# Kernel optimization log

Measured on AMD Instinct MI355X. Metric: run time of the kernel, lower is better.

## Reference

```python
import jax, jax.numpy as jnp
import numpy as np

HIDDEN = [256, 128, 64, 32]
N_IN, N_OUT = 784, 10
V_REST = 0.0; V_RESET = 0.0; V_TH = 1.0; R_MEM = 1.0; DT = 1.0; TAU = 2.0
ALPHA = DT / TAU
SLOPE = 5.0
B, T = 128, 500


def setup_inputs() -> dict:
    key = jax.random.key(0)
    ks = jax.random.split(key, 7)
    sizes = [N_IN] + HIDDEN + [N_OUT]
    inp = {"input_spikes": jax.random.uniform(ks[0], (B, N_IN, T), dtype=jnp.float32)}
    for i in range(len(sizes) - 1):  # 5 weight matrices
        inp[f"w{i}"] = jax.random.uniform(ks[i + 1], (sizes[i], sizes[i + 1]), dtype=jnp.float32) * 0.1
    return inp


def _lif(v, cur):
    # voltage update, surrogate spike, hard reset (reset uses detached spike)
    v = v + (-(v - V_REST) + R_MEM * cur) * ALPHA
    s = jax.nn.sigmoid(SLOPE * (v - V_TH))
    sd = jax.lax.stop_gradient(s)
    v = v * (1.0 - sd) + V_RESET * sd
    return v, s


def reference(input_spikes, w0, w1, w2, w3, w4):
    ws = [jax.nn.relu(w) for w in (w0, w1, w2, w3, w4)]
    n_h = len(HIDDEN)
    b = input_spikes.shape[0]
    dt = input_spikes.dtype
    xs = jnp.transpose(input_spikes, (2, 0, 1))  # (T, B, N_IN)

    v0 = tuple(jnp.full((b, h), V_REST, dtype=dt) for h in HIDDEN)
    v_out0 = jnp.full((b, N_OUT), V_REST, dtype=dt)
    s_prev0 = tuple(jnp.zeros((b, h), dtype=dt) for h in HIDDEN)

    def step(carry, x_t):
        vs, v_out, s_prev = carry
        new_vs, new_s = [], []
        # layer 0 driven by current-step input
        v, s = _lif(vs[0], x_t @ ws[0])
        new_vs.append(v); new_s.append(s)
        # deeper hidden layers driven by PREVIOUS-step spikes (s_prev)
        for li in range(1, n_h):
            v, s = _lif(vs[li], s_prev[li - 1] @ ws[li])
            new_vs.append(v); new_s.append(s)
        # output layer driven by previous-step spikes of last hidden layer
        v_out, s_out = _lif(v_out, s_prev[-1] @ ws[-1])
        return (tuple(new_vs), v_out, tuple(new_s)), (tuple(new_s), s_out)

    _, (hs, outs) = jax.lax.scan(step, (v0, v_out0, s_prev0), xs)
    hidden_spikes = tuple(jnp.transpose(h, (1, 2, 0)) for h in hs)  # each (B, H, T)
    output_spikes = jnp.transpose(outs, (1, 2, 0))                   # (B, N_OUT, T)
    firing_rates = output_spikes.mean(axis=2)                         # (B, N_OUT)
    return (*hidden_spikes, output_spikes, firing_rates)
```

## Files before the change

### kernel.cpp

```cpp
#include <hip/hip_runtime.h>

#define NIN 784
#define H0 256
#define H1 128
#define H2 64
#define H3 32
#define NOUT 10
#define BATCH 128
#define TT 500
#define KCH0 25
#define JTILES 16

#define SW1 136
#define SW2 72
#define SW3 40
#define CW1 132
#define CW2 68
#define CW3 36
#define CW4 20

#define H1_OFF (BATCH * H0 * TT)
#define H2_OFF (H1_OFF + BATCH * H1 * TT)
#define H3_OFF (H2_OFF + BATCH * H2 * TT)
#define OUT_OFF (H3_OFF + BATCH * H3 * TT)
#define RATE_OFF (OUT_OFF + BATCH * NOUT * TT)

typedef __attribute__((ext_vector_type(8))) short short8v;
typedef __attribute__((ext_vector_type(4))) float f32x4;

__device__ __forceinline__ unsigned short f2bf(float f) {
  union { float f; unsigned u; } v; v.f = f;
  unsigned r = v.u + 0x7FFFu + ((v.u >> 16) & 1u);
  return (unsigned short)(r >> 16);
}
__device__ __forceinline__ float bf2f(unsigned short b) {
  union { unsigned u; float f; } v; v.u = ((unsigned)b) << 16;
  return v.f;
}

__device__ __forceinline__ float lif_step(float& v, float c) {
  v = 0.5f * (v + c);
  const float E = __expf(5.0f * (1.0f - v));
  const float r = 1.0f / (1.0f + E);
  v = v * E * r;
  return r;
}

__global__ void pack_all(const float* __restrict__ w0, const float* __restrict__ w1,
                         const float* __restrict__ w2, const float* __restrict__ w3,
                         const float* __restrict__ w4, unsigned short* __restrict__ Wf,
                         unsigned short* __restrict__ Bf) {
  const int bid = blockIdx.x, l = threadIdx.x;
  if (bid < JTILES * KCH0) {
    const int jt = bid / KCH0, kc = bid % KCH0;
    const int j = jt * 16 + (l & 15);
    const int kbase = kc * 32 + (l >> 4) * 8;
    unsigned v[4];
#pragma unroll
    for (int e = 0; e < 4; ++e) {
      const int k0 = kbase + e * 2;
      const float f0 = (k0 < NIN) ? fmaxf(w0[(size_t)k0 * H0 + j], 0.0f) : 0.0f;
      const float f1 = (k0 + 1 < NIN) ? fmaxf(w0[(size_t)(k0 + 1) * H0 + j], 0.0f) : 0.0f;
      v[e] = (unsigned)f2bf(f0) | ((unsigned)f2bf(f1) << 16);
    }
    uint4 o; o.x = v[0]; o.y = v[1]; o.z = v[2]; o.w = v[3];
    reinterpret_cast<uint4*>(Wf)[(size_t)bid * 64 + l] = o;
    return;
  }
  const int tile = bid - JTILES * KCH0;
  const float* w; int K, Nw, base, rel, KCH;
  if (tile < 64)      { w = w1; K = 256; Nw = 128; base = 0;        rel = tile;      KCH = 8; }
  else if (tile < 80) { w = w2; K = 128; Nw = 64;  base = 64 * 512; rel = tile - 64; KCH = 4; }
  else if (tile < 84) { w = w3; K = 64;  Nw = 32;  base = 80 * 512; rel = tile - 80; KCH = 2; }
  else                { w = w4; K = 32;  Nw = 10;  base = 84 * 512; rel = 0;         KCH = 1; }
  const int nt = rel / KCH, kc = rel % KCH;
  const int n = nt * 16 + (l & 15);
  const int kb = kc * 32 + (l >> 4) * 8;
  unsigned v[4];
#pragma unroll
  for (int e = 0; e < 4; ++e) {
    const int k0 = kb + e * 2;
    const float f0 = (n < Nw && k0 < K)     ? fmaxf(w[(size_t)k0 * Nw + n], 0.0f) : 0.0f;
    const float f1 = (n < Nw && k0 + 1 < K) ? fmaxf(w[(size_t)(k0 + 1) * Nw + n], 0.0f) : 0.0f;
    v[e] = (unsigned)f2bf(f0) | ((unsigned)f2bf(f1) << 16);
  }
  uint4 o; o.x = v[0]; o.y = v[1]; o.z = v[2]; o.w = v[3];
  *reinterpret_cast<uint4*>(Bf + base + ((size_t)rel * 64 + l) * 8) = o;
}

__global__ __launch_bounds__(256, 4) void gemm0(
    const float* __restrict__ X, const unsigned short* __restrict__ Wf,
    unsigned short* __restrict__ cur0) {
  const int ttile = blockIdx.x;
  const int b = blockIdx.y;
  const int tid = threadIdx.x;
  const int wave = tid >> 6, lane = tid & 63;
  const int t0 = ttile * 64;
  __shared__ unsigned short Xs[2][64 * 40];
  f32x4 acc[4][4];
#pragma unroll
  for (int i = 0; i < 4; ++i)
#pragma unroll
    for (int jj = 0; jj < 4; ++jj) acc[i][jj] = (f32x4)0.0f;

  const float* Xb = X + (size_t)b * NIN * TT;
  const int tt = tid & 63;
  const int kb = wave * 2;
  const int lrow = lane & 15, lgrp = lane >> 4;
  const int tgl = t0 + tt;
  const bool tin = tgl < TT;

  float r[8];
#pragma unroll
  for (int pp = 0; pp < 4; ++pp) {
    const int k = kb + pp * 8;
    r[pp * 2]     = tin ? Xb[(size_t)k * TT + tgl] : 0.0f;
    r[pp * 2 + 1] = tin ? Xb[(size_t)(k + 1) * TT + tgl] : 0.0f;
  }

  for (int kc = 0; kc < KCH0; ++kc) {
    unsigned short* xbuf = Xs[kc & 1];
#pragma unroll
    for (int pp = 0; pp < 4; ++pp) {
      const unsigned pk = (unsigned)f2bf(r[pp * 2]) | ((unsigned)f2bf(r[pp * 2 + 1]) << 16);
      *reinterpret_cast<unsigned*>(&xbuf[tt * 40 + kb + pp * 8]) = pk;
    }
    __syncthreads();
    if (kc + 1 < KCH0) {
      const int k0 = (kc + 1) * 32;
#pragma unroll
      for (int pp = 0; pp < 4; ++pp) {
        const int k = k0 + kb + pp * 8;
        r[pp * 2]     = (tin && k < NIN)     ? Xb[(size_t)k * TT + tgl] : 0.0f;
        r[pp * 2 + 1] = (tin && k + 1 < NIN) ? Xb[(size_t)(k + 1) * TT + tgl] : 0.0f;
      }
    }
    short8v afr[4], bfr[4];
#pragma unroll
    for (int jf = 0; jf < 4; ++jf) {
      const size_t off = ((size_t)((wave * 4 + jf) * KCH0 + kc) * 64 + lane) * 8;
      afr[jf] = *reinterpret_cast<const short8v*>(Wf + off);
    }
#pragma unroll
    for (int tf = 0; tf < 4; ++tf)
      bfr[tf] = *reinterpret_cast<const short8v*>(&xbuf[(tf * 16 + lrow) * 40 + lgrp * 8]);
#pragma unroll
    for (int jf = 0; jf < 4; ++jf)
#pragma unroll
      for (int tf = 0; tf < 4; ++tf)
        acc[jf][tf] = __builtin_amdgcn_mfma_f32_16x16x32_bf16(afr[jf], bfr[tf], acc[jf][tf], 0, 0, 0);
    __syncthreads();
  }

#pragma unroll
  for (int tf = 0; tf < 4; ++tf) {
    const int t = t0 + tf * 16 + lrow;
    if (t >= TT) continue;
    unsigned short* row = cur0 + ((size_t)b * TT + t) * H0;
#pragma unroll
    for (int jf = 0; jf < 4; ++jf) {
      const int j = wave * 64 + jf * 16 + lgrp * 4;
      const f32x4 a = acc[jf][tf];
      const unsigned p0 = (unsigned)f2bf(a[0]) | ((unsigned)f2bf(a[1]) << 16);
      const unsigned p1 = (unsigned)f2bf(a[2]) | ((unsigned)f2bf(a[3]) << 16);
      *reinterpret_cast<unsigned*>(row + j) = p0;
      *reinterpret_cast<unsigned*>(row + j + 2) = p1;
    }
  }
}

__global__ __launch_bounds__(64) void scan0(
    const unsigned short* __restrict__ cur0, unsigned short* __restrict__ s0g,
    float* __restrict__ out) {
  const int b = blockIdx.y, jg = blockIdx.x, l = threadIdx.x;
  const int j = jg * 64 + l;
  const unsigned short* cp = cur0 + (size_t)b * TT * H0 + j;
  unsigned short* sp = s0g + (size_t)b * 512 * H0 + j;
  float* hp = out + ((size_t)b * H0 + j) * TT;
  sp[0] = 0;
  float v = 0.0f;
  float c0[16], c1[16];
#define LOAD16(D, T0) _Pragma("unroll") for (int u = 0; u < 16; ++u) (D)[u] = bf2f(cp[(size_t)((T0) + u) * H0]);
#define PROC16(C, T0)                                                                \
  do {                                                                               \
    float hb[16];                                                                    \
    _Pragma("unroll")                                                                \
    for (int u = 0; u < 16; ++u) {                                                   \
      const float s = lif_step(v, (C)[u]);                                           \
      hb[u] = s;                                                                     \
      sp[(size_t)((T0) + u + 1) * H0] = f2bf(s);                                     \
    }                                                                                \
    _Pragma("unroll")                                                                \
    for (int q = 0; q < 4; ++q)                                                      \
      *reinterpret_cast<float4*>(hp + (T0) + q * 4) =                                \
          make_float4(hb[q * 4], hb[q * 4 + 1], hb[q * 4 + 2], hb[q * 4 + 3]);       \
  } while (0)
  LOAD16(c0, 0);
  for (int i = 0; i < 15; ++i) {
    const int tb = i * 32;
    LOAD16(c1, tb + 16);
    PROC16(c0, tb);
    LOAD16(c0, tb + 32);
    PROC16(c1, tb + 16);
  }
  PROC16(c0, 480);
  {
    float c[4], hb[4];
#pragma unroll
    for (int u = 0; u < 4; ++u) c[u] = bf2f(cp[(size_t)(496 + u) * H0]);
#pragma unroll
    for (int u = 0; u < 4; ++u) {
      const float s = lif_step(v, c[u]);
      hb[u] = s;
      sp[(size_t)(496 + u + 1) * H0] = f2bf(s);
    }
    *reinterpret_cast<float4*>(hp + 496) = make_float4(hb[0], hb[1], hb[2], hb[3]);
  }
#undef LOAD16
#undef PROC16
}

template<int N>
__device__ __forceinline__ void lif_dynb(float& v, float& rate, const unsigned short* cur,
                                         int cw, unsigned short* sd, int sw, float* hp,
                                         bool wsf) {
  float cr[16];
  const unsigned short* cp = cur;
#pragma unroll
  for (int u = 0; u < N; ++u) { cr[u] = bf2f(*cp); cp += cw; }
  float hb[16];
  unsigned short* sp = sd;
#pragma unroll
  for (int u = 0; u < N; ++u) {
    const float s = lif_step(v, cr[u]);
    hb[u] = s;
    if (wsf) *sp = f2bf(s);
    sp += sw;
    rate += s;
  }
#pragma unroll
  for (int q = 0; q < N / 4; ++q)
    *reinterpret_cast<float4*>(hp + q * 4) =
        make_float4(hb[q * 4], hb[q * 4 + 1], hb[q * 4 + 2], hb[q * 4 + 3]);
}

__global__ __launch_bounds__(512, 1) void snn_tail14(
    const unsigned short* __restrict__ s0g, const unsigned short* __restrict__ Bf,
    float* __restrict__ out) {
  __shared__ __align__(16) unsigned short wl[85 * 512];
  __shared__ __align__(16) unsigned short s1b[65 * SW1];
  __shared__ __align__(16) unsigned short s2b[65 * SW2];
  __shared__ __align__(16) unsigned short s3b[65 * SW3];
  __shared__ __align__(16) unsigned short c1b[64 * CW1];
  __shared__ __align__(16) unsigned short c2b[64 * CW2];
  __shared__ __align__(16) unsigned short c3b[64 * CW3];
  __shared__ __align__(16) unsigned short c4b[64 * CW4];

  const int b = blockIdx.x, tid = threadIdx.x;
  const int w = tid >> 6, lane = tid & 63, lr = lane & 15, lg = lane >> 4;
  const unsigned short* WL1 = wl;
  const unsigned short* WL2 = wl + 64 * 512;
  const unsigned short* WL3 = wl + 80 * 512;
  const unsigned short* WL4 = wl + 84 * 512;
  const unsigned short* s0b = s0g + (size_t)b * 512 * H0;

  {
    const uint4* src = reinterpret_cast<const uint4*>(Bf);
    uint4* dst = reinterpret_cast<uint4*>(wl);
    for (int i = tid; i < 85 * 512 / 8; i += 512) dst[i] = src[i];
  }

  float v = 0.0f, rate = 0.0f;
  int lay = 0, j = 0;
  const unsigned short* curb = nullptr;
  unsigned short* sb = s3b;
  float* hbase = nullptr;
  int cw = 0, sw = 0;
  bool wsf = false, sact = false;
  if (tid < 128) {
    lay = 1; j = tid; curb = c1b + j; sb = s1b; cw = CW1; sw = SW1; wsf = true;
    sact = true; hbase = out + H1_OFF + ((size_t)b * H1 + j) * TT;
  } else if (tid < 192) {
    lay = 2; j = tid - 128; curb = c2b + j; sb = s2b; cw = CW2; sw = SW2; wsf = true;
    sact = true; hbase = out + H2_OFF + ((size_t)b * H2 + j) * TT;
  } else if (tid < 224) {
    lay = 3; j = tid - 192; curb = c3b + j; sb = s3b; cw = CW3; sw = SW3; wsf = true;
    sact = true; hbase = out + H3_OFF + ((size_t)b * H3 + j) * TT;
  } else if (tid < 240) {
    lay = 4; j = tid - 224; curb = c4b + j; sb = s3b; cw = CW4; sw = 0; wsf = false;
    sact = (j < NOUT); hbase = out + OUT_OFF + ((size_t)b * NOUT + j) * TT;
  }
  __syncthreads();

  for (int p = 0; p < 12; ++p) {
    short8v a1[8];
    if (p <= 7) {
      const int tt = w >> 1;
      const unsigned short* ap = s0b + (size_t)(p * 64 + tt * 16 + lr) * H0 + lg * 8;
#pragma unroll
      for (int kc = 0; kc < 8; ++kc) a1[kc] = *reinterpret_cast<const short8v*>(ap + kc * 32);
    }
    if (sact) {
      const int c = p - lay;
      if (c >= 0 && c <= 7) {
        if (wsf) sb[j] = (c == 0) ? (unsigned short)0 : sb[64 * sw + j];
        float* hp = hbase + c * 64;
        unsigned short* sbj = sb + j;
        if (c < 7) {
#pragma unroll
          for (int q = 0; q < 4; ++q)
            lif_dynb<16>(v, rate, curb + q * 16 * cw, cw, sbj + (q * 16 + 1) * sw, sw,
                         hp + q * 16, wsf);
        } else {
          lif_dynb<16>(v, rate, curb, cw, sbj + 1 * sw, sw, hp, wsf);
          lif_dynb<16>(v, rate, curb + 16 * cw, cw, sbj + 17 * sw, sw, hp + 16, wsf);
          lif_dynb<16>(v, rate, curb + 32 * cw, cw, sbj + 33 * sw, sw, hp + 32, wsf);
          lif_dynb<4>(v, rate, curb + 48 * cw, cw, sbj + 49 * sw, sw, hp + 48, wsf);
        }
      }
    }
    __syncthreads();
    if (p <= 7) {
      const int tt = w >> 1, nb = (w & 1) * 4;
#pragma unroll
      for (int n4 = 0; n4 < 4; ++n4) {
        const int nt = nb + n4;
        f32x4 acc = (f32x4)0.0f;
#pragma unroll
        for (int kc = 0; kc < 8; ++kc) {
          const short8v bf = *reinterpret_cast<const short8v*>(WL1 + ((size_t)(nt * 8 + kc) * 64 + lane) * 8);
          acc = __builtin_amdgcn_mfma_f32_16x16x32_bf16(a1[kc], bf, acc, 0, 0, 0);
        }
        unsigned short* cd = c1b + (tt * 16 + lg * 4) * CW1 + nt * 16 + lr;
#pragma unroll
        for (int r = 0; r < 4; ++r) cd[r * CW1] = f2bf(acc[r]);
      }
    }
    if (p >= 1 && p <= 8) {
      const int tt = w >> 1;
      short8v a[4];
      const unsigned short* ap = s1b + (tt * 16 + lr) * SW1 + lg * 8;
#pragma unroll
      for (int kc = 0; kc < 4; ++kc) a[kc] = *reinterpret_cast<const short8v*>(ap + kc * 32);
#pragma unroll
      for (int qi = 0; qi < 2; ++qi) {
        const int nt = (w & 1) * 2 + qi;
        f32x4 acc = (f32x4)0.0f;
#pragma unroll
        for (int kc = 0; kc < 4; ++kc) {
          const short8v bf = *reinterpret_cast<const short8v*>(WL2 + ((size_t)(nt * 4 + kc) * 64 + lane) * 8);
          acc = __builtin_amdgcn_mfma_f32_16x16x32_bf16(a[kc], bf, acc, 0, 0, 0);
        }
        unsigned short* cd = c2b + (tt * 16 + lg * 4) * CW2 + nt * 16 + lr;
#pragma unroll
        for (int r = 0; r < 4; ++r) cd[r * CW2] = f2bf(acc[r]);
      }
    }
    if (p >= 2 && p <= 9) {
      const int tt = w >> 1, nt = w & 1;
      short8v a[2];
      const unsigned short* ap = s2b + (tt * 16 + lr) * SW2 + lg * 8;
#pragma unroll
      for (int kc = 0; kc < 2; ++kc) a[kc] = *reinterpret_cast<const short8v*>(ap + kc * 32);
      f32x4 acc = (f32x4)0.0f;
#pragma unroll
      for (int kc = 0; kc < 2; ++kc) {
        const short8v bf = *reinterpret_cast<const short8v*>(WL3 + ((size_t)(nt * 2 + kc) * 64 + lane) * 8);
        acc = __builtin_amdgcn_mfma_f32_16x16x32_bf16(a[kc], bf, acc, 0, 0, 0);
      }
      unsigned short* cd = c3b + (tt * 16 + lg * 4) * CW3 + nt * 16 + lr;
#pragma unroll
      for (int r = 0; r < 4; ++r) cd[r * CW3] = f2bf(acc[r]);
    }
    if (p >= 3 && p <= 10 && w < 4) {
      const int tt = w;
      const unsigned short* ap = s3b + (tt * 16 + lr) * SW3 + lg * 8;
      const short8v a0 = *reinterpret_cast<const short8v*>(ap);
      const short8v bf = *reinterpret_cast<const short8v*>(WL4 + (size_t)lane * 8);
      f32x4 acc = (f32x4)0.0f;
      acc = __builtin_amdgcn_mfma_f32_16x16x32_bf16(a0, bf, acc, 0, 0, 0);
      unsigned short* cd = c4b + (tt * 16 + lg * 4) * CW4 + lr;
#pragma unroll
      for (int r = 0; r < 4; ++r) cd[r * CW4] = f2bf(acc[r]);
    }
    __syncthreads();
  }
  if (tid >= 224 && tid < 224 + NOUT)
    out[RATE_OFF + (size_t)b * NOUT + (tid - 224)] = rate * (1.0f / (float)TT);
}

extern "C" void kernel_launch(void* const* d_in, const int* in_sizes, int n_in,
                              void* d_out, int out_size, void* d_ws, size_t ws_size,
                              hipStream_t stream) {
  const float* X  = (const float*)d_in[0];
  const float* w0 = (const float*)d_in[1];
  const float* w1 = (const float*)d_in[2];
  const float* w2 = (const float*)d_in[3];
  const float* w3 = (const float*)d_in[4];
  const float* w4 = (const float*)d_in[5];
  float* out = (float*)d_out;

  uint8_t* ws = (uint8_t*)d_ws;
  const size_t SLOT = 33554432;
  unsigned short* cur0 = (unsigned short*)ws;
  unsigned short* s0g  = (unsigned short*)(ws + SLOT);
  unsigned short* Wf0  = (unsigned short*)(ws + 2 * SLOT);
  unsigned short* Bf2  = Wf0 + (size_t)JTILES * KCH0 * 64 * 8;

  pack_all<<<JTILES * KCH0 + 85, 64, 0, stream>>>(w0, w1, w2, w3, w4, Wf0, Bf2);
  gemm0<<<dim3(8, BATCH), 256, 0, stream>>>(X, Wf0, cur0);
  scan0<<<dim3(4, BATCH), 64, 0, stream>>>(cur0, s0g, out);
  snn_tail14<<<BATCH, 512, 0, stream>>>(s0g, Bf2, out);
}
```

Before: 218.2 us.

## Stage tail-layer spikes in LDS and write outputs cooperatively with coalesced stores

Before, the LIF threads for layers 1-4 each wrote their own spike history straight to global memory as float4 runs along the time axis. Those writes were serialized per thread and poorly coalesced across a wave. Now the LIF threads write bf16 spikes only to shared memory, with a new o4b buffer for the output layer. After the matmul phase, all 8 waves copy the staged spikes to global memory, with lanes indexing consecutive timesteps so each store is coalesced. The cost is extra LDS reads, a one-chunk delay in output writes, and output values rounded through bf16; spikes are sigmoid values, so this may change output precision.

Result: faster. 190.1 us (-12.9%).

```diff
diff --git a/kernel.cpp b/kernel.cpp
--- a/kernel.cpp
+++ b/kernel.cpp
@@ -18,6 +18,7 @@
 #define CW2 68
 #define CW3 36
 #define CW4 20
+#define OW4 12
 
 #define H1_OFF (BATCH * H0 * TT)
 #define H2_OFF (H1_OFF + BATCH * H1 * TT)
@@ -221,27 +222,18 @@
 }
 
 template<int N>
-__device__ __forceinline__ void lif_dynb(float& v, float& rate, const unsigned short* cur,
-                                         int cw, unsigned short* sd, int sw, float* hp,
-                                         bool wsf) {
+__device__ __forceinline__ void lif_lds(float& v, float& rate, const unsigned short* cur,
+                                        int cw, unsigned short* sd, int sw) {
   float cr[16];
   const unsigned short* cp = cur;
 #pragma unroll
   for (int u = 0; u < N; ++u) { cr[u] = bf2f(*cp); cp += cw; }
-  float hb[16];
-  unsigned short* sp = sd;
 #pragma unroll
   for (int u = 0; u < N; ++u) {
     const float s = lif_step(v, cr[u]);
-    hb[u] = s;
-    if (wsf) *sp = f2bf(s);
-    sp += sw;
+    *sd = f2bf(s); sd += sw;
     rate += s;
   }
-#pragma unroll
-  for (int q = 0; q < N / 4; ++q)
-    *reinterpret_cast<float4*>(hp + q * 4) =
-        make_float4(hb[q * 4], hb[q * 4 + 1], hb[q * 4 + 2], hb[q * 4 + 3]);
 }
 
 __global__ __launch_bounds__(512, 1) void snn_tail14(
@@ -255,6 +247,7 @@
   __shared__ __align__(16) unsigned short c2b[64 * CW2];
   __shared__ __align__(16) unsigned short c3b[64 * CW3];
   __shared__ __align__(16) unsigned short c4b[64 * CW4];
+  __shared__ __align__(16) unsigned short o4b[64 * OW4];
 
   const int b = blockIdx.x, tid = threadIdx.x;
   const int w = tid >> 6, lane = tid & 63, lr = lane & 15, lg = lane >> 4;
@@ -274,21 +267,21 @@
   int lay = 0, j = 0;
   const unsigned short* curb = nullptr;
   unsigned short* sb = s3b;
-  float* hbase = nullptr;
   int cw = 0, sw = 0;
-  bool wsf = false, sact = false;
+  bool srow0 = false, sact = false;
+  unsigned short* sdbase = nullptr;
   if (tid < 128) {
-    lay = 1; j = tid; curb = c1b + j; sb = s1b; cw = CW1; sw = SW1; wsf = true;
-    sact = true; hbase = out + H1_OFF + ((size_t)b * H1 + j) * TT;
+    lay = 1; j = tid; curb = c1b + j; sb = s1b; cw = CW1; sw = SW1;
+    srow0 = true; sact = true; sdbase = s1b + j + SW1;
   } else if (tid < 192) {
-    lay = 2; j = tid - 128; curb = c2b + j; sb = s2b; cw = CW2; sw = SW2; wsf = true;
-    sact = true; hbase = out + H2_OFF + ((size_t)b * H2 + j) * TT;
+    lay = 2; j = tid - 128; curb = c2b + j; sb = s2b; cw = CW2; sw = SW2;
+    srow0 = true; sact = true; sdbase = s2b + j + SW2;
   } else if (tid < 224) {
-    lay = 3; j = tid - 192; curb = c3b + j; sb = s3b; cw = CW3; sw = SW3; wsf = true;
-    sact = true; hbase = out + H3_OFF + ((size_t)b * H3 + j) * TT;
+    lay = 3; j = tid - 192; curb = c3b + j; sb = s3b; cw = CW3; sw = SW3;
+    srow0 = true; sact = true; sdbase = s3b + j + SW3;
   } else if (tid < 240) {
-    lay = 4; j = tid - 224; curb = c4b + j; sb = s3b; cw = CW4; sw = 0; wsf = false;
-    sact = (j < NOUT); hbase = out + OUT_OFF + ((size_t)b * NOUT + j) * TT;
+    lay = 4; j = tid - 224; curb = c4b + j; cw = CW4; sw = OW4;
+    srow0 = false; sact = (j < NOUT); sdbase = o4b + j;
   }
   __syncthreads();
 
@@ -303,19 +296,16 @@
     if (sact) {
       const int c = p - lay;
       if (c >= 0 && c <= 7) {
-        if (wsf) sb[j] = (c == 0) ? (unsigned short)0 : sb[64 * sw + j];
-        float* hp = hbase + c * 64;
-        unsigned short* sbj = sb + j;
+        if (srow0) sb[j] = (c == 0) ? (unsigned short)0 : sb[64 * sw + j];
         if (c < 7) {
 #pragma unroll
           for (int q = 0; q < 4; ++q)
-            lif_dynb<16>(v, rate, curb + q * 16 * cw, cw, sbj + (q * 16 + 1) * sw, sw,
-                         hp + q * 16, wsf);
+            lif_lds<16>(v, rate, curb + q * 16 * cw, cw, sdbase + q * 16 * sw, sw);
         } else {
-          lif_dynb<16>(v, rate, curb, cw, sbj + 1 * sw, sw, hp, wsf);
-          lif_dynb<16>(v, rate, curb + 16 * cw, cw, sbj + 17 * sw, sw, hp + 16, wsf);
-          lif_dynb<16>(v, rate, curb + 32 * cw, cw, sbj + 33 * sw, sw, hp + 32, wsf);
-          lif_dynb<4>(v, rate, curb + 48 * cw, cw, sbj + 49 * sw, sw, hp + 48, wsf);
+          lif_lds<16>(v, rate, curb, cw, sdbase, sw);
+          lif_lds<16>(v, rate, curb + 16 * cw, cw, sdbase + 16 * sw, sw);
+          lif_lds<16>(v, rate, curb + 32 * cw, cw, sdbase + 32 * sw, sw);
+          lif_lds<4>(v, rate, curb + 48 * cw, cw, sdbase + 48 * sw, sw);
         }
       }
     }
@@ -382,6 +372,48 @@
       unsigned short* cd = c4b + (tt * 16 + lg * 4) * CW4 + lr;
 #pragma unroll
       for (int r = 0; r < 4; ++r) cd[r * CW4] = f2bf(acc[r]);
+    }
+    if (p >= 1 && p <= 8) {
+      const int c = p - 1;
+      const int nt = (c == 7) ? 52 : 64;
+      if (lane < nt) {
+        float* o1 = out + H1_OFF + ((size_t)b * H1 + w * 16) * TT + c * 64 + lane;
+#pragma unroll
+        for (int rr = 0; rr < 16; ++rr)
+          o1[(size_t)rr * TT] = bf2f(s1b[(lane + 1) * SW1 + w * 16 + rr]);
+      }
+    }
+    if (p >= 2 && p <= 9) {
+      const int c = p - 2;
+      const int nt = (c == 7) ? 52 : 64;
+      if (lane < nt) {
+        float* o2 = out + H2_OFF + ((size_t)b * H2 + w * 8) * TT + c * 64 + lane;
+#pragma unroll
+        for (int rr = 0; rr < 8; ++rr)
+          o2[(size_t)rr * TT] = bf2f(s2b[(lane + 1) * SW2 + w * 8 + rr]);
+      }
+    }
+    if (p >= 3 && p <= 10) {
+      const int c = p - 3;
+      const int nt = (c == 7) ? 52 : 64;
+      if (lane < nt) {
+        float* o3 = out + H3_OFF + ((size_t)b * H3 + w * 4) * TT + c * 64 + lane;
+#pragma unroll
+        for (int rr = 0; rr < 4; ++rr)
+          o3[(size_t)rr * TT] = bf2f(s3b[(lane + 1) * SW3 + w * 4 + rr]);
+      }
+    }
+    if (p >= 4 && p <= 11 && w < 5) {
+      const int c = p - 4;
+      const int nt = (c == 7) ? 52 : 64;
+      if (lane < nt) {
+#pragma unroll
+        for (int rr = 0; rr < 2; ++rr) {
+          const int jj = w * 2 + rr;
+          out[OUT_OFF + ((size_t)b * NOUT + jj) * TT + c * 64 + lane] =
+              bf2f(o4b[lane * OW4 + jj]);
+        }
+      }
     }
     __syncthreads();
   }
```
